# Kernel tuning notes

Measured on AMD Instinct MI355X. Metric: run time of the kernel, lower is better.

The kernel has to match this reference:

```python
import jax, jax.numpy as jnp
import numpy as np

N_NODES = 50000
N_EDGES = 800000
IN_F = 128
OUT_F = 128
HEADS = 8
HEAD_DIM = OUT_F // HEADS
EDGE_F = 64


def setup_inputs() -> dict:
    key = jax.random.key(0)
    ks = jax.random.split(key, 12)
    s = 0.05
    return {
        "node_features": jax.random.normal(ks[0], (N_NODES, IN_F), jnp.float32),
        "edge_index": jax.random.randint(ks[1], (2, N_EDGES), 0, N_NODES, jnp.int32),
        "edge_features": jax.random.normal(ks[2], (N_EDGES, EDGE_F), jnp.float32),
        "Wq": jax.random.normal(ks[3], (IN_F, OUT_F), jnp.float32) * s,
        "bq": jnp.zeros((OUT_F,), jnp.float32),
        "Wk": jax.random.normal(ks[4], (IN_F, OUT_F), jnp.float32) * s,
        "bk": jnp.zeros((OUT_F,), jnp.float32),
        "Wv": jax.random.normal(ks[5], (IN_F, OUT_F), jnp.float32) * s,
        "bv": jnp.zeros((OUT_F,), jnp.float32),
        "We": jax.random.normal(ks[6], (EDGE_F, HEADS), jnp.float32) * s,
        "be": jnp.zeros((HEADS,), jnp.float32),
        "Wo": jax.random.normal(ks[7], (OUT_F, OUT_F), jnp.float32) * s,
        "bo": jnp.zeros((OUT_F,), jnp.float32),
    }


def reference(node_features, edge_index, edge_features,
              Wq, bq, Wk, bk, Wv, bv, We, be, Wo, bo):
    n_nodes = node_features.shape[0]
    scale = HEAD_DIM ** (-0.5)
    sources = edge_index[0]
    targets = edge_index[1]

    q = (node_features @ Wq + bq).reshape(n_nodes, HEADS, HEAD_DIM)
    k = (node_features @ Wk + bk).reshape(n_nodes, HEADS, HEAD_DIM)
    v = (node_features @ Wv + bv).reshape(n_nodes, HEADS, HEAD_DIM)

    # edge-wise gathers: [E, H, D]
    q_t = q[targets]
    k_s = k[sources]
    v_s = v[sources]

    # scores [E, H] with edge bias
    scores = jnp.sum(q_t * k_s, axis=-1) * scale + (edge_features @ We + be)

    # segment softmax over edges sharing a target node
    max_s = jax.ops.segment_max(scores, targets, num_segments=n_nodes)
    e = jnp.exp(scores - max_s[targets])
    denom = jax.ops.segment_sum(e, targets, num_segments=n_nodes) + 1e-10
    probs = e / denom[targets]

    weighted = (probs[:, :, None] * v_s).reshape(scores.shape[0], -1)  # [E, H*D]
    agg = jax.ops.segment_sum(weighted, targets, num_segments=n_nodes)  # [N, H*D]
    return agg @ Wo + bo
```

## Files before the change

kernel.cpp:

```cpp
#include <hip/hip_runtime.h>
#include <hip/hip_bf16.h>
#include <math.h>

#define IN_F   128
#define OUT_F  128
#define HEADS  8
#define HEAD_D 16
#define EDGE_F 64
#define BUCKET 64

typedef __attribute__((ext_vector_type(8))) short bf16x8;
typedef __attribute__((ext_vector_type(4))) float f32x4;

__device__ inline unsigned int f2bf(float f) {
    union { float f; unsigned int u; } c; c.f = f;
    unsigned int r = c.u + 0x7FFFu + ((c.u >> 16) & 1u);
    return r >> 16;
}

__global__ __launch_bounds__(256)
void wprep_kernel(const float* __restrict__ Wq, const float* __restrict__ Wk,
                  const float* __restrict__ Wv, const float* __restrict__ Wo,
                  uint4* __restrict__ Wb) {
    int id = blockIdx.x * 256 + threadIdx.x;
    if (id >= 8192) return;
    int lane = id & 63;
    int kb   = (id >> 6) & 3;
    int ct   = (id >> 8) & 7;
    int mat  = id >> 11;
    const float* W = (mat == 0) ? Wq : (mat == 1) ? Wk : (mat == 2) ? Wv : Wo;
    int n  = ct * 16 + (lane & 15);
    int k0 = kb * 32 + (lane >> 4) * 8;
    unsigned int t[8];
    #pragma unroll
    for (int j = 0; j < 8; ++j) t[j] = f2bf(W[(size_t)(k0 + j) * 128 + n]);
    uint4 val;
    val.x = t[0] | (t[1] << 16);
    val.y = t[2] | (t[3] << 16);
    val.z = t[4] | (t[5] << 16);
    val.w = t[6] | (t[7] << 16);
    Wb[id] = val;
}

__global__ __launch_bounds__(256)
void qkv_mfma(const float* __restrict__ x, const bf16x8* __restrict__ WbV,
              const float* __restrict__ bq, const float* __restrict__ bk,
              const float* __restrict__ bv,
              float* __restrict__ q, unsigned int* __restrict__ kvp, int n_nodes) {
    const int tid  = threadIdx.x;
    const int wave = tid >> 6;
    const int lane = tid & 63;
    const int quad = lane >> 4;
    const int lcol = lane & 15;
    const int row0 = blockIdx.x * 64 + wave * 16;
    const int m    = row0 + lcol;

    bf16x8 afrag[4];
    const bool mv = (m < n_nodes);
    const float* xr = x + (size_t)m * IN_F;
    #pragma unroll
    for (int kb = 0; kb < 4; ++kb) {
        float buf[8];
        if (mv) {
            float4 a = ((const float4*)(xr + kb * 32 + quad * 8))[0];
            float4 b = ((const float4*)(xr + kb * 32 + quad * 8 + 4))[0];
            buf[0]=a.x; buf[1]=a.y; buf[2]=a.z; buf[3]=a.w;
            buf[4]=b.x; buf[5]=b.y; buf[6]=b.z; buf[7]=b.w;
        } else {
            #pragma unroll
            for (int j = 0; j < 8; ++j) buf[j] = 0.f;
        }
        bf16x8 f;
        #pragma unroll
        for (int j = 0; j < 8; ++j) f[j] = (short)f2bf(buf[j]);
        afrag[kb] = f;
    }

    #pragma unroll
    for (int ct = 0; ct < 8; ++ct) {
        f32x4 aq = {0.f,0.f,0.f,0.f}, ak = {0.f,0.f,0.f,0.f}, av = {0.f,0.f,0.f,0.f};
        #pragma unroll
        for (int kb = 0; kb < 4; ++kb) {
            bf16x8 bq_ = WbV[((0 * 8 + ct) * 4 + kb) * 64 + lane];
            bf16x8 bk_ = WbV[((1 * 8 + ct) * 4 + kb) * 64 + lane];
            bf16x8 bv_ = WbV[((2 * 8 + ct) * 4 + kb) * 64 + lane];
            aq = __builtin_amdgcn_mfma_f32_16x16x32_bf16(afrag[kb], bq_, aq, 0, 0, 0);
            ak = __builtin_amdgcn_mfma_f32_16x16x32_bf16(afrag[kb], bk_, ak, 0, 0, 0);
            av = __builtin_amdgcn_mfma_f32_16x16x32_bf16(afrag[kb], bv_, av, 0, 0, 0);
        }
        const int col = ct * 16 + lcol;
        float bqc = bq[col], bkc = bk[col], bvc = bv[col];
        #pragma unroll
        for (int r = 0; r < 4; ++r) {
            int node = row0 + quad * 4 + r;
            if (node < n_nodes) {
                size_t o = (size_t)node * OUT_F + col;
                q[o]   = aq[r] + bqc;
                kvp[o] = f2bf(ak[r] + bkc) | (f2bf(av[r] + bvc) << 16);
            }
        }
    }
}

__global__ __launch_bounds__(256)
void ebias_kernel(const float* __restrict__ ef,
                  const float* __restrict__ We, const float* __restrict__ be,
                  float* __restrict__ ebias, int n_edges) {
    __shared__ float sWe[EDGE_F * HEADS];
    __shared__ float sbe[HEADS];
    const int tid = threadIdx.x;
    for (int i = tid; i < EDGE_F * HEADS; i += 256) sWe[i] = We[i];
    if (tid < HEADS) sbe[tid] = be[tid];
    __syncthreads();

    const int e = blockIdx.x * 256 + tid;
    if (e >= n_edges) return;

    float acc[HEADS];
    #pragma unroll
    for (int h = 0; h < HEADS; ++h) acc[h] = sbe[h];

    const float4* er = (const float4*)(ef + (size_t)e * EDGE_F);
    #pragma unroll
    for (int j4 = 0; j4 < EDGE_F / 4; ++j4) {
        float4 evv = er[j4];
        float ev[4] = {evv.x, evv.y, evv.z, evv.w};
        #pragma unroll
        for (int jj = 0; jj < 4; ++jj) {
            int j = j4 * 4 + jj;
            #pragma unroll
            for (int h = 0; h < HEADS; ++h)
                acc[h] = fmaf(ev[jj], sWe[j * HEADS + h], acc[h]);
        }
    }
    float4* dst = (float4*)(ebias + (size_t)e * HEADS);
    dst[0] = make_float4(acc[0], acc[1], acc[2], acc[3]);
    dst[1] = make_float4(acc[4], acc[5], acc[6], acc[7]);
}

__global__ __launch_bounds__(256)
void scatter_kernel(const int* __restrict__ ei, int* __restrict__ deg,
                    int2* __restrict__ csr2, int n_edges) {
    int e = blockIdx.x * 256 + threadIdx.x;
    if (e < n_edges) {
        int s = ei[e];
        int t = ei[n_edges + e];
        int pos = atomicAdd(&deg[t], 1);
        if (pos < BUCKET) csr2[((size_t)t << 6) + pos] = make_int2(s, e);
    }
}

__global__ __launch_bounds__(128)
void agg_kernel(const int2* __restrict__ csr2, const int* __restrict__ deg,
                const float* __restrict__ q, const unsigned int* __restrict__ kvp,
                const float* __restrict__ ebias, unsigned short* __restrict__ aggn) {
    const int t   = blockIdx.x;
    const int tid = threadIdx.x;
    const int h   = tid >> 4;
    const float qj = q[(size_t)t * OUT_F + tid];

    const int beg = t << 6;
    int cnt = deg[t]; if (cnt > BUCKET) cnt = BUCKET;
    const int end = beg + cnt;

    float acc = 0.f, den = 0.f;

    unsigned int kvw0 = 0, kvw1 = 0;
    float eb0 = 0.f, eb1 = 0.f;
    if (beg < end) {
        int2 se = csr2[beg];
        kvw0 = kvp[(size_t)se.x * OUT_F + tid];
        eb0  = ebias[(size_t)se.y * HEADS + h];
    }
    if (beg + 1 < end) {
        int2 se = csr2[beg + 1];
        kvw1 = kvp[(size_t)se.x * OUT_F + tid];
        eb1  = ebias[(size_t)se.y * HEADS + h];
    }

    int i = beg;
    while (i + 1 < end) {
        unsigned int nkv0 = 0, nkv1 = 0;
        float neb0 = 0.f, neb1 = 0.f;
        if (i + 2 < end) {
            int2 se = csr2[i + 2];
            nkv0 = kvp[(size_t)se.x * OUT_F + tid];
            neb0 = ebias[(size_t)se.y * HEADS + h];
        }
        if (i + 3 < end) {
            int2 se = csr2[i + 3];
            nkv1 = kvp[(size_t)se.x * OUT_F + tid];
            neb1 = ebias[(size_t)se.y * HEADS + h];
        }
        {
            float kf = __uint_as_float(kvw0 << 16);
            float vf = __uint_as_float(kvw0 & 0xFFFF0000u);
            float p = qj * kf;
            p += __shfl_xor(p, 8, 16);
            p += __shfl_xor(p, 4, 16);
            p += __shfl_xor(p, 2, 16);
            p += __shfl_xor(p, 1, 16);
            float w = __expf(fmaf(p, 0.25f, eb0));
            den += w;
            acc = fmaf(w, vf, acc);
        }
        {
            float kf = __uint_as_float(kvw1 << 16);
            float vf = __uint_as_float(kvw1 & 0xFFFF0000u);
            float p = qj * kf;
            p += __shfl_xor(p, 8, 16);
            p += __shfl_xor(p, 4, 16);
            p += __shfl_xor(p, 2, 16);
            p += __shfl_xor(p, 1, 16);
            float w = __expf(fmaf(p, 0.25f, eb1));
            den += w;
            acc = fmaf(w, vf, acc);
        }
        kvw0 = nkv0; eb0 = neb0;
        kvw1 = nkv1; eb1 = neb1;
        i += 2;
    }
    if (i < end) {
        float kf = __uint_as_float(kvw0 << 16);
        float vf = __uint_as_float(kvw0 & 0xFFFF0000u);
        float p = qj * kf;
        p += __shfl_xor(p, 8, 16);
        p += __shfl_xor(p, 4, 16);
        p += __shfl_xor(p, 2, 16);
        p += __shfl_xor(p, 1, 16);
        float w = __expf(fmaf(p, 0.25f, eb0));
        den += w;
        acc = fmaf(w, vf, acc);
    }
    aggn[(size_t)t * OUT_F + tid] = (unsigned short)f2bf(acc / (den + 1e-10f));
}

__global__ __launch_bounds__(256)
void out_mfma(const unsigned short* __restrict__ aggn, const bf16x8* __restrict__ WbV,
              const float* __restrict__ bo, float* __restrict__ out, int n_nodes) {
    const int tid  = threadIdx.x;
    const int wave = tid >> 6;
    const int lane = tid & 63;
    const int quad = lane >> 4;
    const int lcol = lane & 15;
    const int row0 = blockIdx.x * 64 + wave * 16;
    const int m    = row0 + lcol;

    bf16x8 afrag[4];
    const bool mv = (m < n_nodes);
    const bf16x8* ar = (const bf16x8*)(aggn + (size_t)m * OUT_F);
    #pragma unroll
    for (int kb = 0; kb < 4; ++kb) {
        if (mv) afrag[kb] = ar[kb * 4 + quad];
        else {
            bf16x8 z;
            #pragma unroll
            for (int j = 0; j < 8; ++j) z[j] = 0;
            afrag[kb] = z;
        }
    }

    #pragma unroll
    for (int ct = 0; ct < 8; ++ct) {
        f32x4 acc = {0.f, 0.f, 0.f, 0.f};
        #pragma unroll
        for (int kb = 0; kb < 4; ++kb) {
            bf16x8 b = WbV[((3 * 8 + ct) * 4 + kb) * 64 + lane];
            acc = __builtin_amdgcn_mfma_f32_16x16x32_bf16(afrag[kb], b, acc, 0, 0, 0);
        }
        const int col = ct * 16 + lcol;
        float boc = bo[col];
        #pragma unroll
        for (int r = 0; r < 4; ++r) {
            int node = row0 + quad * 4 + r;
            if (node < n_nodes) out[(size_t)node * OUT_F + col] = acc[r] + boc;
        }
    }
}

extern "C" void kernel_launch(void* const* d_in, const int* in_sizes, int n_in,
                              void* d_out, int out_size, void* d_ws, size_t ws_size,
                              hipStream_t stream) {
    const float* x  = (const float*)d_in[0];
    const int*   ei = (const int*)  d_in[1];
    const float* ef = (const float*)d_in[2];
    const float* Wq = (const float*)d_in[3];
    const float* bq = (const float*)d_in[4];
    const float* Wk = (const float*)d_in[5];
    const float* bk = (const float*)d_in[6];
    const float* Wv = (const float*)d_in[7];
    const float* bv = (const float*)d_in[8];
    const float* We = (const float*)d_in[9];
    const float* be = (const float*)d_in[10];
    const float* Wo = (const float*)d_in[11];
    const float* bo = (const float*)d_in[12];
    float* out = (float*)d_out;

    const int n_nodes = in_sizes[0] / IN_F;
    const int n_edges = in_sizes[1] / 2;

    char* w = (char*)d_ws;
    float*          q     = (float*)w;          w += (size_t)n_nodes * OUT_F * 4;
    unsigned int*   kvp   = (unsigned int*)w;   w += (size_t)n_nodes * OUT_F * 4;
    float*          ebias = (float*)w;          w += (size_t)n_edges * HEADS * 4;
    unsigned short* aggn  = (unsigned short*)w; w += (size_t)n_nodes * OUT_F * 2;
    uint4*          Wb    = (uint4*)w;          w += (size_t)8192 * 16;
    int*            deg   = (int*)w;            w += (size_t)n_nodes * 4;
    int2*           csr2  = (int2*)w;

    hipMemsetAsync(deg, 0, (size_t)n_nodes * sizeof(int), stream);

    wprep_kernel<<<32, 256, 0, stream>>>(Wq, Wk, Wv, Wo, Wb);

    qkv_mfma<<<(n_nodes + 63) / 64, 256, 0, stream>>>(
        x, (const bf16x8*)Wb, bq, bk, bv, q, kvp, n_nodes);

    ebias_kernel<<<(n_edges + 255) / 256, 256, 0, stream>>>(ef, We, be, ebias, n_edges);

    scatter_kernel<<<(n_edges + 255) / 256, 256, 0, stream>>>(ei, deg, csr2, n_edges);

    agg_kernel<<<n_nodes, 128, 0, stream>>>(csr2, deg, q, kvp, ebias, aggn);

    out_mfma<<<(n_nodes + 63) / 64, 256, 0, stream>>>(aggn, (const bf16x8*)Wb, bo, out, n_nodes);
}
```

Measured before the change: 514.5 us.

## Merge ebias, scatter and QKV kernels into one launch; deepen agg prefetch

Folds the edge-bias, CSR scatter and QKV MFMA kernels into a single block-partitioned launch, so the three independent stages can run at the same time and two launch gaps go away. The aggregation kernel now stages each node's bucket of (source, edge) pairs in shared memory and keeps an 8-deep register ring of in-flight gathers, up from 2, to hide gather latency. The trade-off is higher register use in agg_kernel, a shared-memory staging step with a barrier, and a branchy fused kernel whose shared memory is allocated to every block.

After: 640.4 us. 24.5% more time.

```diff
diff --git a/kernel.cpp b/kernel.cpp
--- a/kernel.cpp
+++ b/kernel.cpp
@@ -8,6 +8,7 @@
 #define HEAD_D 16
 #define EDGE_F 64
 #define BUCKET 64
+#define AGG_D  8
 
 typedef __attribute__((ext_vector_type(8))) short bf16x8;
 typedef __attribute__((ext_vector_type(4))) float f32x4;
@@ -43,110 +44,113 @@
 }
 
 __global__ __launch_bounds__(256)
-void qkv_mfma(const float* __restrict__ x, const bf16x8* __restrict__ WbV,
-              const float* __restrict__ bq, const float* __restrict__ bk,
-              const float* __restrict__ bv,
-              float* __restrict__ q, unsigned int* __restrict__ kvp, int n_nodes) {
-    const int tid  = threadIdx.x;
-    const int wave = tid >> 6;
-    const int lane = tid & 63;
-    const int quad = lane >> 4;
-    const int lcol = lane & 15;
-    const int row0 = blockIdx.x * 64 + wave * 16;
-    const int m    = row0 + lcol;
-
-    bf16x8 afrag[4];
-    const bool mv = (m < n_nodes);
-    const float* xr = x + (size_t)m * IN_F;
-    #pragma unroll
-    for (int kb = 0; kb < 4; ++kb) {
-        float buf[8];
-        if (mv) {
-            float4 a = ((const float4*)(xr + kb * 32 + quad * 8))[0];
-            float4 b = ((const float4*)(xr + kb * 32 + quad * 8 + 4))[0];
-            buf[0]=a.x; buf[1]=a.y; buf[2]=a.z; buf[3]=a.w;
-            buf[4]=b.x; buf[5]=b.y; buf[6]=b.z; buf[7]=b.w;
-        } else {
-            #pragma unroll
-            for (int j = 0; j < 8; ++j) buf[j] = 0.f;
-        }
-        bf16x8 f;
-        #pragma unroll
-        for (int j = 0; j < 8; ++j) f[j] = (short)f2bf(buf[j]);
-        afrag[kb] = f;
-    }
-
-    #pragma unroll
-    for (int ct = 0; ct < 8; ++ct) {
-        f32x4 aq = {0.f,0.f,0.f,0.f}, ak = {0.f,0.f,0.f,0.f}, av = {0.f,0.f,0.f,0.f};
+void phase1_kernel(const float* __restrict__ x, const int* __restrict__ ei,
+                   const float* __restrict__ ef,
+                   const float* __restrict__ We, const float* __restrict__ be,
+                   const bf16x8* __restrict__ WbV,
+                   const float* __restrict__ bq, const float* __restrict__ bk,
+                   const float* __restrict__ bv,
+                   float* __restrict__ q, unsigned int* __restrict__ kvp,
+                   float* __restrict__ ebias, int* __restrict__ deg,
+                   int2* __restrict__ csr2,
+                   int n_nodes, int n_edges, int nbE, int nbS) {
+    const int b   = blockIdx.x;
+    const int tid = threadIdx.x;
+
+    if (b < nbE) {
+        __shared__ float sWe[EDGE_F * HEADS];
+        __shared__ float sbe[HEADS];
+        for (int i = tid; i < EDGE_F * HEADS; i += 256) sWe[i] = We[i];
+        if (tid < HEADS) sbe[tid] = be[tid];
+        __syncthreads();
+
+        const int e = b * 256 + tid;
+        if (e >= n_edges) return;
+
+        float acc[HEADS];
+        #pragma unroll
+        for (int h = 0; h < HEADS; ++h) acc[h] = sbe[h];
+
+        const float4* er = (const float4*)(ef + (size_t)e * EDGE_F);
+        #pragma unroll
+        for (int j4 = 0; j4 < EDGE_F / 4; ++j4) {
+            float4 evv = er[j4];
+            float ev[4] = {evv.x, evv.y, evv.z, evv.w};
+            #pragma unroll
+            for (int jj = 0; jj < 4; ++jj) {
+                int j = j4 * 4 + jj;
+                #pragma unroll
+                for (int h = 0; h < HEADS; ++h)
+                    acc[h] = fmaf(ev[jj], sWe[j * HEADS + h], acc[h]);
+            }
+        }
+        float4* dst = (float4*)(ebias + (size_t)e * HEADS);
+        dst[0] = make_float4(acc[0], acc[1], acc[2], acc[3]);
+        dst[1] = make_float4(acc[4], acc[5], acc[6], acc[7]);
+
+    } else if (b < nbE + nbS) {
+        int e = (b - nbE) * 256 + tid;
+        if (e < n_edges) {
+            int s = ei[e];
+            int t = ei[n_edges + e];
+            int pos = atomicAdd(&deg[t], 1);
+            if (pos < BUCKET) csr2[((size_t)t << 6) + pos] = make_int2(s, e);
+        }
+
+    } else {
+        const int qb   = b - nbE - nbS;
+        const int wave = tid >> 6;
+        const int lane = tid & 63;
+        const int quad = lane >> 4;
+        const int lcol = lane & 15;
+        const int row0 = qb * 64 + wave * 16;
+        const int m    = row0 + lcol;
+
+        bf16x8 afrag[4];
+        const bool mv = (m < n_nodes);
+        const float* xr = x + (size_t)m * IN_F;
         #pragma unroll
         for (int kb = 0; kb < 4; ++kb) {
-            bf16x8 bq_ = WbV[((0 * 8 + ct) * 4 + kb) * 64 + lane];
-            bf16x8 bk_ = WbV[((1 * 8 + ct) * 4 + kb) * 64 + lane];
-            bf16x8 bv_ = WbV[((2 * 8 + ct) * 4 + kb) * 64 + lane];
-            aq = __builtin_amdgcn_mfma_f32_16x16x32_bf16(afrag[kb], bq_, aq, 0, 0, 0);
-            ak = __builtin_amdgcn_mfma_f32_16x16x32_bf16(afrag[kb], bk_, ak, 0, 0, 0);
-            av = __builtin_amdgcn_mfma_f32_16x16x32_bf16(afrag[kb], bv_, av, 0, 0, 0);
-        }
-        const int col = ct * 16 + lcol;
-        float bqc = bq[col], bkc = bk[col], bvc = bv[col];
-        #pragma unroll
-        for (int r = 0; r < 4; ++r) {
-            int node = row0 + quad * 4 + r;
-            if (node < n_nodes) {
-                size_t o = (size_t)node * OUT_F + col;
-                q[o]   = aq[r] + bqc;
-                kvp[o] = f2bf(ak[r] + bkc) | (f2bf(av[r] + bvc) << 16);
-            }
-        }
-    }
-}
-
-__global__ __launch_bounds__(256)
-void ebias_kernel(const float* __restrict__ ef,
-                  const float* __restrict__ We, const float* __restrict__ be,
-                  float* __restrict__ ebias, int n_edges) {
-    __shared__ float sWe[EDGE_F * HEADS];
-    __shared__ float sbe[HEADS];
-    const int tid = threadIdx.x;
-    for (int i = tid; i < EDGE_F * HEADS; i += 256) sWe[i] = We[i];
-    if (tid < HEADS) sbe[tid] = be[tid];
-    __syncthreads();
-
-    const int e = blockIdx.x * 256 + tid;
-    if (e >= n_edges) return;
-
-    float acc[HEADS];
-    #pragma unroll
-    for (int h = 0; h < HEADS; ++h) acc[h] = sbe[h];
-
-    const float4* er = (const float4*)(ef + (size_t)e * EDGE_F);
-    #pragma unroll
-    for (int j4 = 0; j4 < EDGE_F / 4; ++j4) {
-        float4 evv = er[j4];
-        float ev[4] = {evv.x, evv.y, evv.z, evv.w};
-        #pragma unroll
-        for (int jj = 0; jj < 4; ++jj) {
-            int j = j4 * 4 + jj;
-            #pragma unroll
-            for (int h = 0; h < HEADS; ++h)
-                acc[h] = fmaf(ev[jj], sWe[j * HEADS + h], acc[h]);
-        }
-    }
-    float4* dst = (float4*)(ebias + (size_t)e * HEADS);
-    dst[0] = make_float4(acc[0], acc[1], acc[2], acc[3]);
-    dst[1] = make_float4(acc[4], acc[5], acc[6], acc[7]);
-}
-
-__global__ __launch_bounds__(256)
-void scatter_kernel(const int* __restrict__ ei, int* __restrict__ deg,
-                    int2* __restrict__ csr2, int n_edges) {
-    int e = blockIdx.x * 256 + threadIdx.x;
-    if (e < n_edges) {
-        int s = ei[e];
-        int t = ei[n_edges + e];
-        int pos = atomicAdd(&deg[t], 1);
-        if (pos < BUCKET) csr2[((size_t)t << 6) + pos] = make_int2(s, e);
+            float buf[8];
+            if (mv) {
+                float4 a = ((const float4*)(xr + kb * 32 + quad * 8))[0];
+                float4 c = ((const float4*)(xr + kb * 32 + quad * 8 + 4))[0];
+                buf[0]=a.x; buf[1]=a.y; buf[2]=a.z; buf[3]=a.w;
+                buf[4]=c.x; buf[5]=c.y; buf[6]=c.z; buf[7]=c.w;
+            } else {
+                #pragma unroll
+                for (int j = 0; j < 8; ++j) buf[j] = 0.f;
+            }
+            bf16x8 f;
+            #pragma unroll
+            for (int j = 0; j < 8; ++j) f[j] = (short)f2bf(buf[j]);
+            afrag[kb] = f;
+        }
+
+        #pragma unroll
+        for (int ct = 0; ct < 8; ++ct) {
+            f32x4 aq = {0.f,0.f,0.f,0.f}, ak = {0.f,0.f,0.f,0.f}, av = {0.f,0.f,0.f,0.f};
+            #pragma unroll
+            for (int kb = 0; kb < 4; ++kb) {
+                bf16x8 bq_ = WbV[((0 * 8 + ct) * 4 + kb) * 64 + lane];
+                bf16x8 bk_ = WbV[((1 * 8 + ct) * 4 + kb) * 64 + lane];
+                bf16x8 bv_ = WbV[((2 * 8 + ct) * 4 + kb) * 64 + lane];
+                aq = __builtin_amdgcn_mfma_f32_16x16x32_bf16(afrag[kb], bq_, aq, 0, 0, 0);
+                ak = __builtin_amdgcn_mfma_f32_16x16x32_bf16(afrag[kb], bk_, ak, 0, 0, 0);
+                av = __builtin_amdgcn_mfma_f32_16x16x32_bf16(afrag[kb], bv_, av, 0, 0, 0);
+            }
+            const int col = ct * 16 + lcol;
+            float bqc = bq[col], bkc = bk[col], bvc = bv[col];
+            #pragma unroll
+            for (int r = 0; r < 4; ++r) {
+                int node = row0 + quad * 4 + r;
+                if (node < n_nodes) {
+                    size_t o = (size_t)node * OUT_F + col;
+                    q[o]   = aq[r] + bqc;
+                    kvp[o] = f2bf(ak[r] + bkc) | (f2bf(av[r] + bvc) << 16);
+                }
+            }
+        }
     }
 }
 
@@ -157,80 +161,53 @@
     const int t   = blockIdx.x;
     const int tid = threadIdx.x;
     const int h   = tid >> 4;
+
+    __shared__ int2 sed[BUCKET];
+    ((int*)sed)[tid] = ((const int*)(csr2 + ((size_t)t << 6)))[tid];
+
     const float qj = q[(size_t)t * OUT_F + tid];
-
-    const int beg = t << 6;
     int cnt = deg[t]; if (cnt > BUCKET) cnt = BUCKET;
-    const int end = beg + cnt;
+    __syncthreads();
 
     float acc = 0.f, den = 0.f;
 
-    unsigned int kvw0 = 0, kvw1 = 0;
-    float eb0 = 0.f, eb1 = 0.f;
-    if (beg < end) {
-        int2 se = csr2[beg];
-        kvw0 = kvp[(size_t)se.x * OUT_F + tid];
-        eb0  = ebias[(size_t)se.y * HEADS + h];
-    }
-    if (beg + 1 < end) {
-        int2 se = csr2[beg + 1];
-        kvw1 = kvp[(size_t)se.x * OUT_F + tid];
-        eb1  = ebias[(size_t)se.y * HEADS + h];
-    }
-
-    int i = beg;
-    while (i + 1 < end) {
-        unsigned int nkv0 = 0, nkv1 = 0;
-        float neb0 = 0.f, neb1 = 0.f;
-        if (i + 2 < end) {
-            int2 se = csr2[i + 2];
-            nkv0 = kvp[(size_t)se.x * OUT_F + tid];
-            neb0 = ebias[(size_t)se.y * HEADS + h];
-        }
-        if (i + 3 < end) {
-            int2 se = csr2[i + 3];
-            nkv1 = kvp[(size_t)se.x * OUT_F + tid];
-            neb1 = ebias[(size_t)se.y * HEADS + h];
-        }
-        {
-            float kf = __uint_as_float(kvw0 << 16);
-            float vf = __uint_as_float(kvw0 & 0xFFFF0000u);
-            float p = qj * kf;
-            p += __shfl_xor(p, 8, 16);
-            p += __shfl_xor(p, 4, 16);
-            p += __shfl_xor(p, 2, 16);
-            p += __shfl_xor(p, 1, 16);
-            float w = __expf(fmaf(p, 0.25f, eb0));
-            den += w;
-            acc = fmaf(w, vf, acc);
-        }
-        {
-            float kf = __uint_as_float(kvw1 << 16);
-            float vf = __uint_as_float(kvw1 & 0xFFFF0000u);
-            float p = qj * kf;
-            p += __shfl_xor(p, 8, 16);
-            p += __shfl_xor(p, 4, 16);
-            p += __shfl_xor(p, 2, 16);
-            p += __shfl_xor(p, 1, 16);
-            float w = __expf(fmaf(p, 0.25f, eb1));
-            den += w;
-            acc = fmaf(w, vf, acc);
-        }
-        kvw0 = nkv0; eb0 = neb0;
-        kvw1 = nkv1; eb1 = neb1;
-        i += 2;
-    }
-    if (i < end) {
-        float kf = __uint_as_float(kvw0 << 16);
-        float vf = __uint_as_float(kvw0 & 0xFFFF0000u);
-        float p = qj * kf;
-        p += __shfl_xor(p, 8, 16);
-        p += __shfl_xor(p, 4, 16);
-        p += __shfl_xor(p, 2, 16);
-        p += __shfl_xor(p, 1, 16);
-        float w = __expf(fmaf(p, 0.25f, eb0));
-        den += w;
-        acc = fmaf(w, vf, acc);
+    unsigned int kvw[AGG_D];
+    float eb[AGG_D];
+    #pragma unroll
+    for (int j = 0; j < AGG_D; ++j) {
+        kvw[j] = 0; eb[j] = 0.f;
+        if (j < cnt) {
+            int2 se = sed[j];
+            kvw[j] = kvp[(size_t)se.x * OUT_F + tid];
+            eb[j]  = ebias[(size_t)se.y * HEADS + h];
+        }
+    }
+
+    for (int base = 0; base < cnt; base += AGG_D) {
+        #pragma unroll
+        for (int j = 0; j < AGG_D; ++j) {
+            int idx = base + j;
+            if (idx < cnt) {
+                unsigned int w0 = kvw[j];
+                float e0 = eb[j];
+                int nidx = idx + AGG_D;
+                if (nidx < cnt) {
+                    int2 se = sed[nidx];
+                    kvw[j] = kvp[(size_t)se.x * OUT_F + tid];
+                    eb[j]  = ebias[(size_t)se.y * HEADS + h];
+                }
+                float kf = __uint_as_float(w0 << 16);
+                float vf = __uint_as_float(w0 & 0xFFFF0000u);
+                float p = qj * kf;
+                p += __shfl_xor(p, 8, 16);
+                p += __shfl_xor(p, 4, 16);
+                p += __shfl_xor(p, 2, 16);
+                p += __shfl_xor(p, 1, 16);
+                float w = __expf(fmaf(p, 0.25f, e0));
+                den += w;
+                acc = fmaf(w, vf, acc);
+            }
+        }
     }
     aggn[(size_t)t * OUT_F + tid] = (unsigned short)f2bf(acc / (den + 1e-10f));
 }
@@ -312,12 +289,12 @@
 
     wprep_kernel<<<32, 256, 0, stream>>>(Wq, Wk, Wv, Wo, Wb);
 
-    qkv_mfma<<<(n_nodes + 63) / 64, 256, 0, stream>>>(
-        x, (const bf16x8*)Wb, bq, bk, bv, q, kvp, n_nodes);
-
-    ebias_kernel<<<(n_edges + 255) / 256, 256, 0, stream>>>(ef, We, be, ebias, n_edges);
-
-    scatter_kernel<<<(n_edges + 255) / 256, 256, 0, stream>>>(ei, deg, csr2, n_edges);
+    const int nbE = (n_edges + 255) / 256;
+    const int nbS = (n_edges + 255) / 256;
+    const int nbQ = (n_nodes + 63) / 64;
+    phase1_kernel<<<nbE + nbS + nbQ, 256, 0, stream>>>(
+        x, ei, ef, We, be, (const bf16x8*)Wb, bq, bk, bv,
+        q, kvp, ebias, deg, csr2, n_nodes, n_edges, nbE, nbS);
 
     agg_kernel<<<n_nodes, 128, 0, stream>>>(csr2, deg, q, kvp, ebias, aggn);
 
```
